# Kernel tuning notes

Hardware: AMD Instinct MI355X
Metric: run time of the kernel (lower is better)

## Reference

```python
import jax, jax.numpy as jnp
import numpy as np
import math

D_MODEL = 2048
HEADS = 16
D_K = D_MODEL // HEADS
B, S = 4, 2048


def setup_inputs() -> dict:
    key = jax.random.key(0)
    ks = jax.random.split(key, 11)
    scale = 1.0 / math.sqrt(D_MODEL)
    inp = {
        "q": jax.random.normal(ks[0], (B, S, D_MODEL), dtype=jnp.float32),
        "k": jax.random.normal(ks[1], (B, S, D_MODEL), dtype=jnp.float32),
        "v": jax.random.normal(ks[2], (B, S, D_MODEL), dtype=jnp.float32),
        "w_q": jax.random.normal(ks[3], (D_MODEL, D_MODEL), dtype=jnp.float32) * scale,
        "b_q": jnp.zeros((D_MODEL,), dtype=jnp.float32),
        "w_k": jax.random.normal(ks[4], (D_MODEL, D_MODEL), dtype=jnp.float32) * scale,
        "b_k": jnp.zeros((D_MODEL,), dtype=jnp.float32),
        "w_v": jax.random.normal(ks[5], (D_MODEL, D_MODEL), dtype=jnp.float32) * scale,
        "b_v": jnp.zeros((D_MODEL,), dtype=jnp.float32),
        "w_o": jax.random.normal(ks[6], (D_MODEL, D_MODEL), dtype=jnp.float32) * scale,
        "b_o": jnp.zeros((D_MODEL,), dtype=jnp.float32),
    }
    return inp


def reference(q, k, v, w_q, b_q, w_k, b_k, w_v, b_v, w_o, b_o):
    # Linear projections (torch Linear: x @ W^T + b; here W stored pre-transposed)
    query = q @ w_q + b_q  # [B,S,D]
    key = k @ w_k + b_k
    value = v @ w_v + b_v
    # split heads -> [B,H,S,d_k]
    def split(x):
        return x.reshape(B, S, HEADS, D_K).transpose(0, 2, 1, 3)
    qh, kh, vh = split(query), split(key), split(value)
    # scaled dot-product attention (full score matrix, as in original)
    scores = jnp.einsum('bhqd,bhkd->bhqk', qh, kh) / jnp.sqrt(jnp.float32(D_K))
    attn = jax.nn.softmax(scores, axis=-1)
    out = jnp.einsum('bhqk,bhkd->bhqd', attn, vh)  # [B,H,S,d_k]
    out = out.transpose(0, 2, 1, 3).reshape(B, S, D_MODEL)
    return out @ w_o + b_o
```

## Files before the change

kernel.cpp:

```cpp
#include <hip/hip_runtime.h>
#include <hip/hip_bf16.h>

#define DMODEL 2048
#define HEADS 16
#define DK 128
#define BATCH 4
#define SEQ 2048
#define MROWS (BATCH * SEQ)

typedef __attribute__((ext_vector_type(8))) short bf16x8;
typedef __attribute__((ext_vector_type(4))) short bf16x4;
typedef __attribute__((ext_vector_type(4))) float f32x4;
typedef __attribute__((ext_vector_type(16))) float f32x16;

static __device__ __forceinline__ short f2bf(float x) {
    __hip_bfloat16 h = __float2bfloat16(x);
    union { __hip_bfloat16 h; short s; } u;
    u.h = h;
    return u.s;
}

static __device__ __forceinline__ int cvt_pk_bf16(float lo, float hi) {
    int r;
    asm("v_cvt_pk_bf16_f32 %0, %1, %2" : "=v"(r) : "v"(lo), "v"(hi));
    return r;
}

static __device__ __forceinline__ float exp2_fast(float x) {
    float r;
    asm("v_exp_f32 %0, %1" : "=v"(r) : "v"(x));
    return r;
}

#define MFMA16(a, b, c) __builtin_amdgcn_mfma_f32_16x16x32_bf16((a), (b), (c), 0, 0, 0)
#define MFMA32(a, b, c) __builtin_amdgcn_mfma_f32_32x32x16_bf16((a), (b), (c), 0, 0, 0)

static __device__ __forceinline__ void load_lds16(const void* g, void* l) {
    __builtin_amdgcn_global_load_lds(
        (const __attribute__((address_space(1))) unsigned int*)g,
        (__attribute__((address_space(3))) unsigned int*)l, 16, 0, 0);
}

__global__ __launch_bounds__(256) void cvt3_bf16(
    const float* __restrict__ i0, const float* __restrict__ i1,
    const float* __restrict__ i2, short* __restrict__ o0,
    short* __restrict__ o1, short* __restrict__ o2, int n8) {
    int i = blockIdx.x * blockDim.x + threadIdx.x;
    const int stride = gridDim.x * blockDim.x;
    for (; i < 3 * n8; i += stride) {
        const int which = i / n8;
        const int idx = i - which * n8;
        const float* in = which == 0 ? i0 : (which == 1 ? i1 : i2);
        short* out = which == 0 ? o0 : (which == 1 ? o1 : o2);
        f32x4 a = ((const f32x4*)in)[idx * 2];
        f32x4 b = ((const f32x4*)in)[idx * 2 + 1];
        bf16x8 o;
        o[0] = f2bf(a[0]); o[1] = f2bf(a[1]); o[2] = f2bf(a[2]); o[3] = f2bf(a[3]);
        o[4] = f2bf(b[0]); o[5] = f2bf(b[1]); o[6] = f2bf(b[2]); o[7] = f2bf(b[3]);
        ((bf16x8*)out)[idx] = o;
    }
}

__global__ __launch_bounds__(256) void cvt_tr4(
    const float* __restrict__ w0, const float* __restrict__ w1,
    const float* __restrict__ w2, const float* __restrict__ w3,
    short* __restrict__ t0, short* __restrict__ t1,
    short* __restrict__ t2, short* __restrict__ t3) {
    __shared__ short t[64][72];
    const int which = blockIdx.z;
    const float* W = which == 0 ? w0 : (which == 1 ? w1 : (which == 2 ? w2 : w3));
    short* Wt = which == 0 ? t0 : (which == 1 ? t1 : (which == 2 ? t2 : t3));
    const int n0 = blockIdx.x * 64, k0 = blockIdx.y * 64;
    const int tid = threadIdx.x;
#pragma unroll
    for (int p = 0; p < 4; p++) {
        const int kr = p * 16 + (tid >> 4);
        const int nc = (tid & 15) * 4;
        f32x4 v = *(const f32x4*)&W[(size_t)(k0 + kr) * DMODEL + n0 + nc];
#pragma unroll
        for (int j = 0; j < 4; j++) t[nc + j][kr] = f2bf(v[j]);
    }
    __syncthreads();
    const int nr = tid >> 2, ch = (tid & 3) * 16;
    *(bf16x8*)&Wt[(size_t)(n0 + nr) * DMODEL + k0 + ch] = *(const bf16x8*)&t[nr][ch];
    *(bf16x8*)&Wt[(size_t)(n0 + nr) * DMODEL + k0 + ch + 8] = *(const bf16x8*)&t[nr][ch + 8];
}

__global__ __launch_bounds__(256) void tr_bf16(const short* __restrict__ in,
                                               short* __restrict__ out) {
    __shared__ short t[64][65];
    const int c0 = blockIdx.x * 64, r0 = blockIdx.y * 64;
    const int tid = threadIdx.x;
    const int row = tid >> 2, cb = (tid & 3) * 16;
    bf16x8 a = *(const bf16x8*)&in[(size_t)(r0 + row) * DMODEL + c0 + cb];
    bf16x8 b2 = *(const bf16x8*)&in[(size_t)(r0 + row) * DMODEL + c0 + cb + 8];
#pragma unroll
    for (int j = 0; j < 8; j++) { t[cb + j][row] = a[j]; t[cb + 8 + j][row] = b2[j]; }
    __syncthreads();
#pragma unroll
    for (int j = 0; j < 16; j++)
        out[(size_t)(c0 + row) * MROWS + r0 + cb + j] = t[row][cb + j];
}

static __device__ __forceinline__ void stage2(const char* gbase, char* lbase,
                                              int rb, int r8, int scol, int ktb) {
#pragma unroll
    for (int i = 0; i < 2; i++)
        load_lds16(gbase + (size_t)(rb + i * 8 + r8) * (DMODEL * 2) + ktb + scol,
                   lbase + (rb + i * 8) * 128);
}

template <typename OT, bool TRANSV = false>
__global__ __launch_bounds__(512, 2) void gemm8(
    const short* __restrict__ A, const short* __restrict__ Bt,
    const float* __restrict__ bias, OT* __restrict__ C, float oscale) {
    __shared__ short Asl[256 * 64];
    __shared__ short Bsl[256 * 64];
    const int tid = threadIdx.x, lane = tid & 63, wid = tid >> 6;

    const int nwg = gridDim.x;
    const int bid = blockIdx.x;
    const int swz = (bid & 7) * (nwg >> 3) + (bid >> 3);
    const int bx = swz >> 5, by = swz & 31;
    const int row0 = by * 256, col0 = bx * 256;
    const int wm = wid >> 2, wn = wid & 3;

    const int r8 = lane >> 3;
    const int scol = ((lane & 7) * 16) ^ (r8 << 4);
    const int a1r = ((wid & 4) << 5) + (wid & 3) * 16;
    const int b1r = (wid >> 1) * 64 + (wid & 1) * 16;

    const char* Ab = (const char*)A + (size_t)row0 * (DMODEL * 2);
    const char* Bb = (const char*)Bt + (size_t)col0 * (DMODEL * 2);

    const int arow = wm * 128 + (lane & 15);
    const int brow = wn * 64 + (lane & 15);
    const int fg = (lane >> 4) * 16;
    const int fx = (lane & 7) << 4;

    f32x4 acc[8][4] = {};
    bf16x8 af[4][2], bfr[4][2];

    const int NT = DMODEL / 64;

    stage2(Ab, (char*)Asl, a1r, r8, scol, 0);
    stage2(Bb, (char*)Bsl, b1r, r8, scol, 0);
    stage2(Bb, (char*)Bsl, b1r + 32, r8, scol, 0);
    stage2(Ab, (char*)Asl, a1r + 64, r8, scol, 0);

    for (int t = 0; t < NT; t++) {
        const bool more = (t + 1) < NT;
        const int ktb = (t + 1) * 128;

        asm volatile("s_waitcnt vmcnt(4)" ::: "memory");
        asm volatile("s_waitcnt lgkmcnt(0)" ::: "memory");
        __builtin_amdgcn_s_barrier();
        __builtin_amdgcn_sched_barrier(0);
#pragma unroll
        for (int m = 0; m < 4; m++)
#pragma unroll
            for (int kk = 0; kk < 2; kk++)
                af[m][kk] = *(const bf16x8*)((const char*)Asl + (arow + m * 16) * 128 + ((kk * 64 + fg) ^ fx));
#pragma unroll
        for (int n = 0; n < 2; n++)
#pragma unroll
            for (int kk = 0; kk < 2; kk++)
                bfr[n][kk] = *(const bf16x8*)((const char*)Bsl + (brow + n * 16) * 128 + ((kk * 64 + fg) ^ fx));
        __builtin_amdgcn_s_setprio(1);
#pragma unroll
        for (int m = 0; m < 4; m++)
#pragma unroll
            for (int n = 0; n < 2; n++)
#pragma unroll
                for (int kk = 0; kk < 2; kk++)
                    acc[m][n] = MFMA16(af[m][kk], bfr[n][kk], acc[m][n]);
        __builtin_amdgcn_s_setprio(0);

        asm volatile("s_waitcnt vmcnt(2)" ::: "memory");
        asm volatile("s_waitcnt lgkmcnt(0)" ::: "memory");
        __builtin_amdgcn_s_barrier();
        __builtin_amdgcn_sched_barrier(0);
#pragma unroll
        for (int n = 2; n < 4; n++)
#pragma unroll
            for (int kk = 0; kk < 2; kk++)
                bfr[n][kk] = *(const bf16x8*)((const char*)Bsl + (brow + n * 16) * 128 + ((kk * 64 + fg) ^ fx));
        if (more) {
            stage2(Ab, (char*)Asl, a1r, r8, scol, ktb);
            stage2(Bb, (char*)Bsl, b1r, r8, scol, ktb);
        }
        __builtin_amdgcn_s_setprio(1);
#pragma unroll
        for (int m = 0; m < 4; m++)
#pragma unroll
            for (int n = 2; n < 4; n++)
#pragma unroll
                for (int kk = 0; kk < 2; kk++)
                    acc[m][n] = MFMA16(af[m][kk], bfr[n][kk], acc[m][n]);
        __builtin_amdgcn_s_setprio(0);

        if (more) asm volatile("s_waitcnt vmcnt(4)" ::: "memory");
        else      asm volatile("s_waitcnt vmcnt(0)" ::: "memory");
        asm volatile("s_waitcnt lgkmcnt(0)" ::: "memory");
        __builtin_amdgcn_s_barrier();
        __builtin_amdgcn_sched_barrier(0);
#pragma unroll
        for (int mi = 0; mi < 4; mi++)
#pragma unroll
            for (int kk = 0; kk < 2; kk++)
                af[mi][kk] = *(const bf16x8*)((const char*)Asl + (arow + 64 + mi * 16) * 128 + ((kk * 64 + fg) ^ fx));
        if (more) stage2(Bb, (char*)Bsl, b1r + 32, r8, scol, ktb);
        __builtin_amdgcn_s_setprio(1);
#pragma unroll
        for (int mi = 0; mi < 4; mi++)
#pragma unroll
            for (int n = 2; n < 4; n++)
#pragma unroll
                for (int kk = 0; kk < 2; kk++)
                    acc[4 + mi][n] = MFMA16(af[mi][kk], bfr[n][kk], acc[4 + mi][n]);
        __builtin_amdgcn_s_setprio(0);

        asm volatile("s_waitcnt lgkmcnt(0)" ::: "memory");
        __builtin_amdgcn_s_barrier();
        __builtin_amdgcn_sched_barrier(0);
        if (more) stage2(Ab, (char*)Asl, a1r + 64, r8, scol, ktb);
        __builtin_amdgcn_s_setprio(1);
#pragma unroll
        for (int mi = 0; mi < 4; mi++)
#pragma unroll
            for (int n = 0; n < 2; n++)
#pragma unroll
                for (int kk = 0; kk < 2; kk++)
                    acc[4 + mi][n] = MFMA16(af[mi][kk], bfr[n][kk], acc[4 + mi][n]);
        __builtin_amdgcn_s_setprio(0);
    }

#pragma unroll
    for (int n = 0; n < 4; n++) {
        const int col = col0 + wn * 64 + n * 16 + (lane & 15);
        const float bz = bias[col];
#pragma unroll
        for (int m = 0; m < 8; m++) {
            const int row4 = row0 + wm * 128 + m * 16 + (lane >> 4) * 4;
            if constexpr (TRANSV) {
                bf16x4 tv;
#pragma unroll
                for (int j = 0; j < 4; j++) tv[j] = f2bf((acc[m][n][j] + bz) * oscale);
                *(bf16x4*)&C[(size_t)col * MROWS + row4] = tv;
            } else {
#pragma unroll
                for (int j = 0; j < 4; j++) {
                    const float v = (acc[m][n][j] + bz) * oscale;
                    if constexpr (sizeof(OT) == 2)
                        C[(size_t)(row4 + j) * DMODEL + col] = (OT)f2bf(v);
                    else
                        C[(size_t)(row4 + j) * DMODEL + col] = (OT)v;
                }
            }
        }
    }
}

template <typename AT, typename OT>
__global__ __launch_bounds__(256) void gemm_kernel(
    const AT* __restrict__ A, const float* __restrict__ W,
    const float* __restrict__ bias, OT* __restrict__ C, float oscale) {
    const int K = DMODEL, N = DMODEL;
    __shared__ short As[128][40];
    __shared__ short Bs[128][40];
    const int tid = threadIdx.x;
    const int lane = tid & 63;
    const int wid = tid >> 6;
    const int wm = wid >> 1, wn = wid & 1;
    const int row0 = blockIdx.y * 128;
    const int col0 = blockIdx.x * 128;
    f32x4 acc[4][4] = {};
    const int a_row = tid >> 1;
    const int a_col = (tid & 1) * 16;
    const int b_n = (tid & 31) * 4;
    const int b_k = (tid >> 5) * 4;
    for (int k0 = 0; k0 < K; k0 += 32) {
        __syncthreads();
        {
            const AT* src = A + (size_t)(row0 + a_row) * K + k0 + a_col;
            if constexpr (sizeof(AT) == 4) {
                const float* sf = reinterpret_cast<const float*>(src);
                f32x4 v0 = *(const f32x4*)(sf + 0);
                f32x4 v1 = *(const f32x4*)(sf + 4);
                f32x4 v2 = *(const f32x4*)(sf + 8);
                f32x4 v3 = *(const f32x4*)(sf + 12);
                bf16x8 w0, w1;
                w0[0] = f2bf(v0[0]); w0[1] = f2bf(v0[1]); w0[2] = f2bf(v0[2]); w0[3] = f2bf(v0[3]);
                w0[4] = f2bf(v1[0]); w0[5] = f2bf(v1[1]); w0[6] = f2bf(v1[2]); w0[7] = f2bf(v1[3]);
                w1[0] = f2bf(v2[0]); w1[1] = f2bf(v2[1]); w1[2] = f2bf(v2[2]); w1[3] = f2bf(v2[3]);
                w1[4] = f2bf(v3[0]); w1[5] = f2bf(v3[1]); w1[6] = f2bf(v3[2]); w1[7] = f2bf(v3[3]);
                *(bf16x8*)&As[a_row][a_col + 0] = w0;
                *(bf16x8*)&As[a_row][a_col + 8] = w1;
            } else {
                const short* ss = reinterpret_cast<const short*>(src);
                *(bf16x8*)&As[a_row][a_col + 0] = *(const bf16x8*)(ss + 0);
                *(bf16x8*)&As[a_row][a_col + 8] = *(const bf16x8*)(ss + 8);
            }
        }
        {
            const float* w0p = W + (size_t)(k0 + b_k + 0) * N + col0 + b_n;
            f32x4 r0 = *(const f32x4*)(w0p);
            f32x4 r1 = *(const f32x4*)(w0p + N);
            f32x4 r2 = *(const f32x4*)(w0p + 2 * N);
            f32x4 r3 = *(const f32x4*)(w0p + 3 * N);
#pragma unroll
            for (int j = 0; j < 4; j++) {
                bf16x4 t;
                t[0] = f2bf(r0[j]); t[1] = f2bf(r1[j]); t[2] = f2bf(r2[j]); t[3] = f2bf(r3[j]);
                *(bf16x4*)&Bs[b_n + j][b_k] = t;
            }
        }
        __syncthreads();
        bf16x8 af[4], bfr[4];
#pragma unroll
        for (int m = 0; m < 4; m++)
            af[m] = *(const bf16x8*)&As[wm * 64 + m * 16 + (lane & 15)][(lane >> 4) * 8];
#pragma unroll
        for (int n = 0; n < 4; n++)
            bfr[n] = *(const bf16x8*)&Bs[wn * 64 + n * 16 + (lane & 15)][(lane >> 4) * 8];
#pragma unroll
        for (int m = 0; m < 4; m++)
#pragma unroll
            for (int n = 0; n < 4; n++)
                acc[m][n] = MFMA16(af[m], bfr[n], acc[m][n]);
    }
#pragma unroll
    for (int m = 0; m < 4; m++) {
#pragma unroll
        for (int n = 0; n < 4; n++) {
            const int col = col0 + wn * 64 + n * 16 + (lane & 15);
            const float bz = bias[col];
#pragma unroll
            for (int j = 0; j < 4; j++) {
                const int row = row0 + wm * 64 + m * 16 + (lane >> 4) * 4 + j;
                const float v = (acc[m][n][j] + bz) * oscale;
                if constexpr (sizeof(OT) == 2)
                    C[(size_t)row * N + col] = (OT)f2bf(v);
                else
                    C[(size_t)row * N + col] = (OT)v;
            }
        }
    }
}

__global__ __launch_bounds__(512, 2) void attn_kernel(
    const short* __restrict__ Qp, const short* __restrict__ Kp,
    const short* __restrict__ Vtp, short* __restrict__ Oout) {
    const int nwg = gridDim.x;
    const int bid = blockIdx.x;
    const int bx = (bid & 7) * (nwg >> 3) + (bid >> 3);
    const int qt = bx & 7;
    const int h = (bx >> 3) & 15;
    const int b = bx >> 7;

    __shared__ short Ks[2][128 * 128];
    __shared__ short Vts[2][128 * 128];

    const int tid = threadIdx.x;
    const int lane = tid & 63;
    const int wid = tid >> 6;
    const int lo = lane & 31;
    const int hi1 = lane >> 5;

    bf16x8 qf[8];
    {
        const short* qrow = Qp + (size_t)(b * SEQ + qt * 256 + wid * 32 + lo) * DMODEL + h * DK;
#pragma unroll
        for (int dk = 0; dk < 8; dk++)
            qf[dk] = *(const bf16x8*)(qrow + dk * 16 + hi1 * 8);
    }

    f32x16 oacc[4] = {};
    float lsum = 0.f;

    const char* Kbase = (const char*)(Kp + (size_t)(b * SEQ) * DMODEL + h * DK);
    const char* Vtbase = (const char*)(Vtp + (size_t)(h * DK) * MROWS + b * SEQ);

    const int srow = wid * 16 + (lane >> 4);
    const int scp = (lane & 15) * 16;
    const int NT = SEQ / 128;
    const float C12 = 17.3123404906676f;

#pragma unroll
    for (int i = 0; i < 4; i++) {
        const int rr = srow + i * 4;
        load_lds16(Kbase + (size_t)rr * (DMODEL * 2) + (scp ^ ((rr & 15) << 4)),
                   (char*)Ks[0] + wid * 4096 + i * 1024);
    }
#pragma unroll
    for (int i = 0; i < 4; i++) {
        const int dd = srow + i * 4;
        load_lds16(Vtbase + (size_t)dd * (MROWS * 2) + (scp ^ ((dd & 15) << 4)),
                   (char*)Vts[0] + wid * 4096 + i * 1024);
    }
    asm volatile("s_waitcnt vmcnt(0)" ::: "memory");
    __builtin_amdgcn_s_barrier();
    __builtin_amdgcn_sched_barrier(0);

    for (int kt = 0; kt < NT; kt++) {
        const int cur = kt & 1;
        const bool more = (kt + 1) < NT;

        if (more) {
#pragma unroll
            for (int i = 0; i < 4; i++) {
                const int rr = srow + i * 4;
                load_lds16(Kbase + (size_t)((kt + 1) * 128 + rr) * (DMODEL * 2) + (scp ^ ((rr & 15) << 4)),
                           (char*)Ks[cur ^ 1] + wid * 4096 + i * 1024);
            }
#pragma unroll
            for (int i = 0; i < 4; i++) {
                const int dd = srow + i * 4;
                load_lds16(Vtbase + (size_t)dd * (MROWS * 2) + (kt + 1) * 256 + (scp ^ ((dd & 15) << 4)),
                           (char*)Vts[cur ^ 1] + wid * 4096 + i * 1024);
            }
        }

        f32x16 sc[2];
        bf16x8 pa[8];

        sc[0] = (f32x16){};
        __builtin_amdgcn_s_setprio(1);
#pragma unroll
        for (int dk = 0; dk < 8; dk++) {
            const int r = 0 * 32 + lo;
            const int cb = (dk * 32 + hi1 * 16) ^ ((r & 15) << 4);
            bf16x8 kf = *(const bf16x8*)((char*)Ks[cur] + r * 256 + cb);
            sc[0] = MFMA32(kf, qf[dk], sc[0]);
        }
        __builtin_amdgcn_s_setprio(0);

#pragma unroll
        for (int g = 0; g < 4; g++) {
            if (g < 3) {
                sc[(g + 1) & 1] = (f32x16){};
                __builtin_amdgcn_s_setprio(1);
#pragma unroll
                for (int dk = 0; dk < 8; dk++) {
                    const int r = (g + 1) * 32 + lo;
                    const int cb = (dk * 32 + hi1 * 16) ^ ((r & 15) << 4);
                    bf16x8 kf = *(const bf16x8*)((char*)Ks[cur] + r * 256 + cb);
                    sc[(g + 1) & 1] = MFMA32(kf, qf[dk], sc[(g + 1) & 1]);
                }
                __builtin_amdgcn_s_setprio(0);
            }
            {
                f32x16& s = sc[g & 1];
#pragma unroll
                for (int r = 0; r < 16; r++)
                    s[r] = exp2_fast(s[r] - C12);
                float s0 = 0.f, s1 = 0.f, s2 = 0.f, s3 = 0.f;
#pragma unroll
                for (int r = 0; r < 16; r += 4) {
                    s0 += s[r]; s1 += s[r + 1]; s2 += s[r + 2]; s3 += s[r + 3];
                }
                lsum += (s0 + s1) + (s2 + s3);
#pragma unroll
                for (int hf = 0; hf < 2; hf++) {
                    const int X0 = cvt_pk_bf16(s[8 * hf + 0], s[8 * hf + 1]);
                    const int X1 = cvt_pk_bf16(s[8 * hf + 2], s[8 * hf + 3]);
                    const int X2 = cvt_pk_bf16(s[8 * hf + 4], s[8 * hf + 5]);
                    const int X3 = cvt_pk_bf16(s[8 * hf + 6], s[8 * hf + 7]);
                    const int L0 = hi1 ? X2 : X0, L1 = hi1 ? X3 : X1;
                    const int S0 = hi1 ? X0 : X2, S1 = hi1 ? X1 : X3;
                    const int R0 = __shfl_xor(S0, 32, 64);
                    const int R1 = __shfl_xor(S1, 32, 64);
                    union { int i[4]; bf16x8 v; } u;
                    u.i[0] = hi1 ? R0 : L0;
                    u.i[1] = hi1 ? R1 : L1;
                    u.i[2] = hi1 ? L0 : R0;
                    u.i[3] = hi1 ? L1 : R1;
                    pa[2 * g + hf] = u.v;
                }
            }
        }

        __builtin_amdgcn_s_setprio(1);
#pragma unroll
        for (int ks = 0; ks < 8; ks++) {
#pragma unroll
            for (int n = 0; n < 4; n++) {
                const int d = n * 32 + lo;
                const int cb = (ks * 32 + hi1 * 16) ^ ((d & 15) << 4);
                bf16x8 vf = *(const bf16x8*)((char*)Vts[cur] + d * 256 + cb);
                oacc[n] = MFMA32(vf, pa[ks], oacc[n]);
            }
        }
        __builtin_amdgcn_s_setprio(0);

        if (more) {
            asm volatile("s_waitcnt vmcnt(0)" ::: "memory");
            asm volatile("s_waitcnt lgkmcnt(0)" ::: "memory");
            __builtin_amdgcn_s_barrier();
            __builtin_amdgcn_sched_barrier(0);
        }
    }

    const float l = lsum + __shfl_xor(lsum, 32, 64);
    const float inv = 1.0f / l;
    short* obase = Oout + (size_t)(b * SEQ + qt * 256 + wid * 32 + lo) * DMODEL + h * DK;
#pragma unroll
    for (int n = 0; n < 4; n++) {
#pragma unroll
        for (int rr = 0; rr < 8; rr++) {
            const int d = n * 32 + 2 * (rr & 1) + 8 * (rr >> 1) + 4 * hi1;
            const int pkv = cvt_pk_bf16(oacc[n][2 * rr] * inv, oacc[n][2 * rr + 1] * inv);
            *(int*)(obase + d) = pkv;
        }
    }
}

extern "C" void kernel_launch(void* const* d_in, const int* in_sizes, int n_in,
                              void* d_out, int out_size, void* d_ws, size_t ws_size,
                              hipStream_t stream) {
    const float* q   = (const float*)d_in[0];
    const float* k   = (const float*)d_in[1];
    const float* v   = (const float*)d_in[2];
    const float* w_q = (const float*)d_in[3];
    const float* b_q = (const float*)d_in[4];
    const float* w_k = (const float*)d_in[5];
    const float* b_k = (const float*)d_in[6];
    const float* w_v = (const float*)d_in[7];
    const float* b_v = (const float*)d_in[8];
    const float* w_o = (const float*)d_in[9];
    const float* b_o = (const float*)d_in[10];
    float* out = (float*)d_out;

    const size_t PROJ = (size_t)MROWS * DMODEL;
    const size_t WSZ = (size_t)DMODEL * DMODEL;
    const float qscale = 0.08838834764831845f * 1.4426950408889634f;
    const int attn_grid = BATCH * HEADS * (SEQ / 256);

    if (ws_size >= (6 * PROJ + 4 * WSZ) * sizeof(short)) {
        short* qbf = (short*)d_ws;
        short* kbf = qbf + PROJ;
        short* vbf = kbf + PROJ;
        short* Qp  = vbf + PROJ;
        short* Kp  = Qp + PROJ;
        short* Vt  = Kp + PROJ;
        short* wtq = Vt + PROJ;
        short* wtk = wtq + WSZ;
        short* wtv = wtk + WSZ;
        short* wto = wtv + WSZ;
        short* Ao  = qbf;

        const int n8 = (int)(PROJ / 8);
        cvt3_bf16<<<3072, 256, 0, stream>>>(q, k, v, qbf, kbf, vbf, n8);
        dim3 gtr(DMODEL / 64, DMODEL / 64, 4);
        cvt_tr4<<<gtr, 256, 0, stream>>>(w_q, w_k, w_v, w_o, wtq, wtk, wtv, wto);

        const int nwg8 = (MROWS / 256) * (DMODEL / 256);
        gemm8<short><<<nwg8, 512, 0, stream>>>(qbf, wtq, b_q, Qp, qscale);
        gemm8<short><<<nwg8, 512, 0, stream>>>(kbf, wtk, b_k, Kp, 1.0f);
        gemm8<short, true><<<nwg8, 512, 0, stream>>>(vbf, wtv, b_v, Vt, 1.0f);

        attn_kernel<<<attn_grid, 512, 0, stream>>>(Qp, Kp, Vt, Ao);

        gemm8<float><<<nwg8, 512, 0, stream>>>(Ao, wto, b_o, out, 1.0f);
    } else {
        short* Qp = (short*)d_ws;
        short* Kp = Qp + PROJ;
        short* Vp = Kp + PROJ;
        short* Vt = Vp + PROJ;
        short* Ao = Vt + PROJ;
        dim3 gblk(DMODEL / 128, MROWS / 128);
        gemm_kernel<float, short><<<gblk, 256, 0, stream>>>(q, w_q, b_q, Qp, qscale);
        gemm_kernel<float, short><<<gblk, 256, 0, stream>>>(k, w_k, b_k, Kp, 1.0f);
        gemm_kernel<float, short><<<gblk, 256, 0, stream>>>(v, w_v, b_v, Vp, 1.0f);
        dim3 gtrv(DMODEL / 64, MROWS / 64);
        tr_bf16<<<gtrv, 256, 0, stream>>>(Vp, Vt);
        attn_kernel<<<attn_grid, 512, 0, stream>>>(Qp, Kp, Vt, Ao);
        gemm_kernel<short, float><<<gblk, 256, 0, stream>>>(Ao, w_o, b_o, out, 1.0f);
    }
}
```

Measured before the change: 543.6 us.

## Double-buffer LDS in projection GEMM with eight-phase ping-pong pipeline

Replaces the single-buffered LDS GEMM with a double-buffered version (two A and two B tiles). Each iteration runs eight phases that issue quarter-tile global-to-LDS prefetches into the other buffer while MFMAs consume the current one, and it reorders the quadrant traversal so B fragments are reused. The staging address mapping is also rewritten. The goal is to overlap global loads with compute more deeply and to reduce stalls at the barriers. In exchange, LDS use doubles to 128KB per workgroup, which may limit the intended two workgroups per CU, and the pipeline has more barriers per K step.

After: 561.5 us. +3.3%, slower.

```diff
diff --git a/kernel.cpp b/kernel.cpp
--- a/kernel.cpp
+++ b/kernel.cpp
@@ -102,20 +102,63 @@
         out[(size_t)(c0 + row) * MROWS + r0 + cb + j] = t[row][cb + j];
 }
 
-static __device__ __forceinline__ void stage2(const char* gbase, char* lbase,
-                                              int rb, int r8, int scol, int ktb) {
-#pragma unroll
-    for (int i = 0; i < 2; i++)
-        load_lds16(gbase + (size_t)(rb + i * 8 + r8) * (DMODEL * 2) + ktb + scol,
-                   lbase + (rb + i * 8) * 128);
-}
+static __device__ __forceinline__ void stageAu(const char* g, char* lds,
+                                               int ro, int ktb, int tid, int wid) {
+#pragma unroll
+    for (int j = 0; j < 2; j++) {
+        const int u = j * 64 + (tid >> 3);
+        const int r = ((u & 63) | ((u >> 6) << 7)) + ro;
+        const int rbase = wid * 8 + j * 128 + ro;
+        load_lds16(g + (size_t)r * (DMODEL * 2) + ktb + (((tid & 7) * 16) ^ ((r & 7) << 4)),
+                   lds + rbase * 128);
+    }
+}
+
+static __device__ __forceinline__ void stageBu(const char* g, char* lds,
+                                               int ro, int ktb, int tid, int wid) {
+#pragma unroll
+    for (int j = 0; j < 2; j++) {
+        const int u = j * 64 + (tid >> 3);
+        const int r = ((u & 31) | ((u >> 5) << 6)) + ro;
+        const int rbase = (wid & 3) * 8 + (j * 2 + (wid >> 2)) * 64 + ro;
+        load_lds16(g + (size_t)r * (DMODEL * 2) + ktb + (((tid & 7) * 16) ^ ((r & 7) << 4)),
+                   lds + rbase * 128);
+    }
+}
+
+#define PHASE_TOP(VMS)                                        \
+    asm volatile("s_waitcnt lgkmcnt(0)" ::: "memory");        \
+    asm volatile("s_waitcnt " VMS ::: "memory");              \
+    __builtin_amdgcn_s_barrier();                             \
+    __builtin_amdgcn_sched_barrier(0);
+
+#define LOAD_AF(buf, mh)                                                          \
+    _Pragma("unroll") for (int mi = 0; mi < 4; mi++)                              \
+    _Pragma("unroll") for (int kk = 0; kk < 2; kk++)                              \
+        af[mi][kk] = *(const bf16x8*)((const char*)Asl[buf] +                     \
+            (wm * 128 + (mh) * 64 + mi * 16 + l15) * 128 + ((kk * 64 + fg) ^ fx));
+
+#define LOAD_BF(dst, buf, nh)                                                     \
+    _Pragma("unroll") for (int ni = 0; ni < 2; ni++)                              \
+    _Pragma("unroll") for (int kk = 0; kk < 2; kk++)                              \
+        dst[ni][kk] = *(const bf16x8*)((const char*)Bsl[buf] +                    \
+            (wn * 64 + (nh) * 32 + ni * 16 + l15) * 128 + ((kk * 64 + fg) ^ fx));
+
+#define MFMA_QUAD(mh, nh, bsrc)                                                   \
+    __builtin_amdgcn_s_setprio(1);                                                \
+    _Pragma("unroll") for (int mi = 0; mi < 4; mi++)                              \
+    _Pragma("unroll") for (int ni = 0; ni < 2; ni++)                              \
+    _Pragma("unroll") for (int kk = 0; kk < 2; kk++)                              \
+        acc[(mh) * 4 + mi][(nh) * 2 + ni] =                                       \
+            MFMA16(af[mi][kk], bsrc[ni][kk], acc[(mh) * 4 + mi][(nh) * 2 + ni]);  \
+    __builtin_amdgcn_s_setprio(0);
 
 template <typename OT, bool TRANSV = false>
-__global__ __launch_bounds__(512, 2) void gemm8(
+__global__ __launch_bounds__(512, 2) void gemm9(
     const short* __restrict__ A, const short* __restrict__ Bt,
     const float* __restrict__ bias, OT* __restrict__ C, float oscale) {
-    __shared__ short Asl[256 * 64];
-    __shared__ short Bsl[256 * 64];
+    __shared__ short Asl[2][256 * 64];
+    __shared__ short Bsl[2][256 * 64];
     const int tid = threadIdx.x, lane = tid & 63, wid = tid >> 6;
 
     const int nwg = gridDim.x;
@@ -125,119 +168,107 @@
     const int row0 = by * 256, col0 = bx * 256;
     const int wm = wid >> 2, wn = wid & 3;
 
-    const int r8 = lane >> 3;
-    const int scol = ((lane & 7) * 16) ^ (r8 << 4);
-    const int a1r = ((wid & 4) << 5) + (wid & 3) * 16;
-    const int b1r = (wid >> 1) * 64 + (wid & 1) * 16;
-
     const char* Ab = (const char*)A + (size_t)row0 * (DMODEL * 2);
     const char* Bb = (const char*)Bt + (size_t)col0 * (DMODEL * 2);
 
-    const int arow = wm * 128 + (lane & 15);
-    const int brow = wn * 64 + (lane & 15);
+    const int l15 = lane & 15;
     const int fg = (lane >> 4) * 16;
     const int fx = (lane & 7) << 4;
 
     f32x4 acc[8][4] = {};
-    bf16x8 af[4][2], bfr[4][2];
-
-    const int NT = DMODEL / 64;
-
-    stage2(Ab, (char*)Asl, a1r, r8, scol, 0);
-    stage2(Bb, (char*)Bsl, b1r, r8, scol, 0);
-    stage2(Bb, (char*)Bsl, b1r + 32, r8, scol, 0);
-    stage2(Ab, (char*)Asl, a1r + 64, r8, scol, 0);
-
-    for (int t = 0; t < NT; t++) {
-        const bool more = (t + 1) < NT;
-        const int ktb = (t + 1) * 128;
-
-        asm volatile("s_waitcnt vmcnt(4)" ::: "memory");
-        asm volatile("s_waitcnt lgkmcnt(0)" ::: "memory");
-        __builtin_amdgcn_s_barrier();
-        __builtin_amdgcn_sched_barrier(0);
-#pragma unroll
-        for (int m = 0; m < 4; m++)
-#pragma unroll
-            for (int kk = 0; kk < 2; kk++)
-                af[m][kk] = *(const bf16x8*)((const char*)Asl + (arow + m * 16) * 128 + ((kk * 64 + fg) ^ fx));
-#pragma unroll
-        for (int n = 0; n < 2; n++)
-#pragma unroll
-            for (int kk = 0; kk < 2; kk++)
-                bfr[n][kk] = *(const bf16x8*)((const char*)Bsl + (brow + n * 16) * 128 + ((kk * 64 + fg) ^ fx));
-        __builtin_amdgcn_s_setprio(1);
-#pragma unroll
-        for (int m = 0; m < 4; m++)
-#pragma unroll
-            for (int n = 0; n < 2; n++)
-#pragma unroll
-                for (int kk = 0; kk < 2; kk++)
-                    acc[m][n] = MFMA16(af[m][kk], bfr[n][kk], acc[m][n]);
-        __builtin_amdgcn_s_setprio(0);
-
-        asm volatile("s_waitcnt vmcnt(2)" ::: "memory");
-        asm volatile("s_waitcnt lgkmcnt(0)" ::: "memory");
-        __builtin_amdgcn_s_barrier();
-        __builtin_amdgcn_sched_barrier(0);
-#pragma unroll
-        for (int n = 2; n < 4; n++)
-#pragma unroll
-            for (int kk = 0; kk < 2; kk++)
-                bfr[n][kk] = *(const bf16x8*)((const char*)Bsl + (brow + n * 16) * 128 + ((kk * 64 + fg) ^ fx));
-        if (more) {
-            stage2(Ab, (char*)Asl, a1r, r8, scol, ktb);
-            stage2(Bb, (char*)Bsl, b1r, r8, scol, ktb);
-        }
-        __builtin_amdgcn_s_setprio(1);
-#pragma unroll
-        for (int m = 0; m < 4; m++)
-#pragma unroll
-            for (int n = 2; n < 4; n++)
-#pragma unroll
-                for (int kk = 0; kk < 2; kk++)
-                    acc[m][n] = MFMA16(af[m][kk], bfr[n][kk], acc[m][n]);
-        __builtin_amdgcn_s_setprio(0);
-
-        if (more) asm volatile("s_waitcnt vmcnt(4)" ::: "memory");
-        else      asm volatile("s_waitcnt vmcnt(0)" ::: "memory");
-        asm volatile("s_waitcnt lgkmcnt(0)" ::: "memory");
-        __builtin_amdgcn_s_barrier();
-        __builtin_amdgcn_sched_barrier(0);
-#pragma unroll
-        for (int mi = 0; mi < 4; mi++)
-#pragma unroll
-            for (int kk = 0; kk < 2; kk++)
-                af[mi][kk] = *(const bf16x8*)((const char*)Asl + (arow + 64 + mi * 16) * 128 + ((kk * 64 + fg) ^ fx));
-        if (more) stage2(Bb, (char*)Bsl, b1r + 32, r8, scol, ktb);
-        __builtin_amdgcn_s_setprio(1);
-#pragma unroll
-        for (int mi = 0; mi < 4; mi++)
-#pragma unroll
-            for (int n = 2; n < 4; n++)
-#pragma unroll
-                for (int kk = 0; kk < 2; kk++)
-                    acc[4 + mi][n] = MFMA16(af[mi][kk], bfr[n][kk], acc[4 + mi][n]);
-        __builtin_amdgcn_s_setprio(0);
-
-        asm volatile("s_waitcnt lgkmcnt(0)" ::: "memory");
-        __builtin_amdgcn_s_barrier();
-        __builtin_amdgcn_sched_barrier(0);
-        if (more) stage2(Ab, (char*)Asl, a1r + 64, r8, scol, ktb);
-        __builtin_amdgcn_s_setprio(1);
-#pragma unroll
-        for (int mi = 0; mi < 4; mi++)
-#pragma unroll
-            for (int n = 0; n < 2; n++)
-#pragma unroll
-                for (int kk = 0; kk < 2; kk++)
-                    acc[4 + mi][n] = MFMA16(af[mi][kk], bfr[n][kk], acc[4 + mi][n]);
-        __builtin_amdgcn_s_setprio(0);
+    bf16x8 af[4][2], bA[2][2], bB[2][2];
+
+    stageAu(Ab, (char*)Asl[0], 0, 0, tid, wid);
+    stageBu(Bb, (char*)Bsl[0], 0, 0, tid, wid);
+    stageBu(Bb, (char*)Bsl[0], 32, 0, tid, wid);
+    stageAu(Ab, (char*)Asl[0], 64, 0, tid, wid);
+    stageAu(Ab, (char*)Asl[1], 0, 128, tid, wid);
+
+    const int NIT = DMODEL / 128;
+    for (int it = 0; it < NIT - 1; it++) {
+        const int o1 = (2 * it + 1) * 128;
+        const int e2 = (2 * it + 2) * 128;
+        const int o2 = (2 * it + 3) * 128;
+
+        PHASE_TOP("vmcnt(6)");
+        LOAD_AF(0, 0); LOAD_BF(bA, 0, 0);
+        stageBu(Bb, (char*)Bsl[1], 0, o1, tid, wid);
+        MFMA_QUAD(0, 0, bA);
+
+        PHASE_TOP("vmcnt(6)");
+        LOAD_BF(bB, 0, 1);
+        stageBu(Bb, (char*)Bsl[1], 32, o1, tid, wid);
+        MFMA_QUAD(0, 1, bB);
+
+        PHASE_TOP("vmcnt(6)");
+        LOAD_AF(0, 1);
+        stageAu(Ab, (char*)Asl[1], 64, o1, tid, wid);
+        MFMA_QUAD(1, 1, bB);
+
+        PHASE_TOP("vmcnt(6)");
+        stageAu(Ab, (char*)Asl[0], 0, e2, tid, wid);
+        MFMA_QUAD(1, 0, bA);
+
+        PHASE_TOP("vmcnt(6)");
+        LOAD_AF(1, 0); LOAD_BF(bA, 1, 0);
+        stageBu(Bb, (char*)Bsl[0], 0, e2, tid, wid);
+        MFMA_QUAD(0, 0, bA);
+
+        PHASE_TOP("vmcnt(6)");
+        LOAD_BF(bB, 1, 1);
+        stageBu(Bb, (char*)Bsl[0], 32, e2, tid, wid);
+        MFMA_QUAD(0, 1, bB);
+
+        PHASE_TOP("vmcnt(6)");
+        LOAD_AF(1, 1);
+        stageAu(Ab, (char*)Asl[0], 64, e2, tid, wid);
+        MFMA_QUAD(1, 1, bB);
+
+        PHASE_TOP("vmcnt(6)");
+        stageAu(Ab, (char*)Asl[1], 0, o2, tid, wid);
+        MFMA_QUAD(1, 0, bA);
+    }
+
+    {
+        const int o1 = (DMODEL / 64 - 1) * 128;
+
+        PHASE_TOP("vmcnt(6)");
+        LOAD_AF(0, 0); LOAD_BF(bA, 0, 0);
+        stageBu(Bb, (char*)Bsl[1], 0, o1, tid, wid);
+        MFMA_QUAD(0, 0, bA);
+
+        PHASE_TOP("vmcnt(6)");
+        LOAD_BF(bB, 0, 1);
+        stageBu(Bb, (char*)Bsl[1], 32, o1, tid, wid);
+        MFMA_QUAD(0, 1, bB);
+
+        PHASE_TOP("vmcnt(6)");
+        LOAD_AF(0, 1);
+        stageAu(Ab, (char*)Asl[1], 64, o1, tid, wid);
+        MFMA_QUAD(1, 1, bB);
+
+        PHASE_TOP("vmcnt(6)");
+        MFMA_QUAD(1, 0, bA);
+
+        PHASE_TOP("vmcnt(4)");
+        LOAD_AF(1, 0); LOAD_BF(bA, 1, 0);
+        MFMA_QUAD(0, 0, bA);
+
+        PHASE_TOP("vmcnt(2)");
+        LOAD_BF(bB, 1, 1);
+        MFMA_QUAD(0, 1, bB);
+
+        PHASE_TOP("vmcnt(0)");
+        LOAD_AF(1, 1);
+        MFMA_QUAD(1, 1, bB);
+
+        PHASE_TOP("vmcnt(0)");
+        MFMA_QUAD(1, 0, bA);
     }
 
 #pragma unroll
     for (int n = 0; n < 4; n++) {
-        const int col = col0 + wn * 64 + n * 16 + (lane & 15);
+        const int col = col0 + wn * 64 + n * 16 + l15;
         const float bz = bias[col];
 #pragma unroll
         for (int m = 0; m < 8; m++) {
@@ -555,13 +586,13 @@
         cvt_tr4<<<gtr, 256, 0, stream>>>(w_q, w_k, w_v, w_o, wtq, wtk, wtv, wto);
 
         const int nwg8 = (MROWS / 256) * (DMODEL / 256);
-        gemm8<short><<<nwg8, 512, 0, stream>>>(qbf, wtq, b_q, Qp, qscale);
-        gemm8<short><<<nwg8, 512, 0, stream>>>(kbf, wtk, b_k, Kp, 1.0f);
-        gemm8<short, true><<<nwg8, 512, 0, stream>>>(vbf, wtv, b_v, Vt, 1.0f);
+        gemm9<short><<<nwg8, 512, 0, stream>>>(qbf, wtq, b_q, Qp, qscale);
+        gemm9<short><<<nwg8, 512, 0, stream>>>(kbf, wtk, b_k, Kp, 1.0f);
+        gemm9<short, true><<<nwg8, 512, 0, stream>>>(vbf, wtv, b_v, Vt, 1.0f);
 
         attn_kernel<<<attn_grid, 512, 0, stream>>>(Qp, Kp, Vt, Ao);
 
-        gemm8<float><<<nwg8, 512, 0, stream>>>(Ao, wto, b_o, out, 1.0f);
+        gemm9<float><<<nwg8, 512, 0, stream>>>(Ao, wto, b_o, out, 1.0f);
     } else {
         short* Qp = (short*)d_ws;
         short* Kp = Qp + PROJ;
```
